# Optimization experiments

Hardware: AMD Instinct MI355X
Metric: run time of the kernel (lower is better)

Reference implementation:

```python
import jax, jax.numpy as jnp
import numpy as np
from jax import lax

SOFTPLUS_THRESHOLD = 20.0

def _softplus_thresh(z):
    # softplus(z, beta=1, threshold=20): linear above threshold
    return jnp.where(z > SOFTPLUS_THRESHOLD, z,
                     jnp.log1p(jnp.exp(jnp.minimum(z, SOFTPLUS_THRESHOLD))))

def setup_inputs() -> dict:
    key = jax.random.key(0)
    ks = jax.random.split(key, 8)
    L, E, R, N = 512, 5120, 160, 16
    scale = 0.02
    x = jax.random.normal(ks[0], (1, 1, L, E), dtype=jnp.float32)
    W_dt_low = jax.random.normal(ks[1], (E, R), dtype=jnp.float32) * scale
    W_dt = jax.random.normal(ks[2], (R, E), dtype=jnp.float32) * scale
    dt_bias = jax.random.normal(ks[3], (E,), dtype=jnp.float32) * scale
    W_B = jax.random.normal(ks[4], (E, N), dtype=jnp.float32) * scale
    W_C = jax.random.normal(ks[5], (E, N), dtype=jnp.float32) * scale
    # A_log ~ log of positive values so A = -exp(A_log) is a stable decay
    A_log = jnp.log(1.0 + jax.random.uniform(ks[6], (E, N), dtype=jnp.float32) * 15.0)
    D = jax.random.normal(ks[7], (E,), dtype=jnp.float32)
    return {"x": x, "W_dt_low": W_dt_low, "W_dt": W_dt, "dt_bias": dt_bias,
            "W_B": W_B, "W_C": W_C, "A_log": A_log, "D": D}

def reference(x, W_dt_low, W_dt, dt_bias, W_B, W_C, A_log, D):
    orig_shape = x.shape              # [1,1,L,E]
    L, E = orig_shape[-2], orig_shape[-1]
    xf = x.reshape(L, E)
    # delta_t: x -> dt_rank -> d_inner, then thresholded softplus
    delta = _softplus_thresh((xf @ W_dt_low) @ W_dt + dt_bias)   # [L,E]
    A = -jnp.exp(A_log)                                          # [E,N]
    # discretization: abar = exp(delta * A), bbar = delta * B * x
    abar = jnp.exp(delta[:, :, None] * A[None])                  # [L,E,N]
    B = xf @ W_B                                                 # [L,N]
    bbar = delta[:, :, None] * B[:, None, :] * xf[:, :, None]    # [L,E,N]
    # linear recurrence h_t = abar_t * h_{t-1} + bbar_t via associative scan
    def combine(c1, c2):
        a1, b1 = c1
        a2, b2 = c2
        return a1 * a2, a2 * b1 + b2
    _, h = lax.associative_scan(combine, (abar, bbar), axis=0)   # [L,E,N]
    C = xf @ W_C                                                 # [L,N]
    y = jnp.einsum('len,ln->le', h, C)                           # hc_sum_reduce
    out = xf * D + y
    return out.reshape(orig_shape)
```

## Files before the change

### kernel.cpp

```cpp
#include <hip/hip_runtime.h>
#include <math.h>

#define LL 512
#define EE 5120
#define RR 160
#define NS 16
#define NTOT 192
#define KS 32
#define KCHUNK 160
#define CH 16
#define NC 32

#define XCONV_BLOCKS 1280
#define WALL_TILES   960
#define WDT_TILES    800

typedef __attribute__((ext_vector_type(8))) short short8;
typedef __attribute__((ext_vector_type(4))) short short4v;
typedef __attribute__((ext_vector_type(4))) float f32x4;

__device__ inline float softplus_t(float z) {
    return z > 20.f ? z : log1pf(__expf(fminf(z, 20.f)));
}

__device__ inline short f2bf(float f) {
    unsigned u = __float_as_uint(f);
    unsigned r = (u + 0x7FFFu + ((u >> 16) & 1u)) >> 16;
    return (short)r;
}

__device__ inline float bf2f(unsigned short u) {
    return __uint_as_float(((unsigned)u) << 16);
}

__global__ __launch_bounds__(256) void prep_kernel(
        const float* __restrict__ x,
        const float* __restrict__ Wlow,
        const float* __restrict__ WB,
        const float* __restrict__ WC,
        const float* __restrict__ Wdt,
        short* __restrict__ xb,
        short* __restrict__ WallT,
        short* __restrict__ WdtT) {
    const int tid = threadIdx.x;
    const int bid = blockIdx.x;
    if (bid < XCONV_BLOCKS) {
        size_t base = (size_t)bid * 2048 + (size_t)tid * 8;
        float4 v0 = *reinterpret_cast<const float4*>(x + base);
        float4 v1 = *reinterpret_cast<const float4*>(x + base + 4);
        short8 o;
        o[0] = f2bf(v0.x); o[1] = f2bf(v0.y); o[2] = f2bf(v0.z); o[3] = f2bf(v0.w);
        o[4] = f2bf(v1.x); o[5] = f2bf(v1.y); o[6] = f2bf(v1.z); o[7] = f2bf(v1.w);
        *reinterpret_cast<short8*>(xb + base) = o;
        return;
    }
    __shared__ float tile[32][33];
    const int row = tid >> 3, col4 = (tid & 7) * 4;
    if (bid < XCONV_BLOCKS + WALL_TILES) {
        const int t = bid - XCONV_BLOCKS;
        const int k0 = (t / 6) * 32, n0 = (t % 6) * 32;
#pragma unroll
        for (int i = 0; i < 4; ++i) {
            int n = n0 + col4 + i, k = k0 + row;
            float v;
            if (n < RR)            v = Wlow[(size_t)k * RR + n];
            else if (n < RR + NS)  v = WB[(size_t)k * NS + (n - RR)];
            else                   v = WC[(size_t)k * NS + (n - RR - NS)];
            tile[row][col4 + i] = v;
        }
        __syncthreads();
        const int nr = tid >> 3, kc = (tid & 7) * 4;
        short4v o;
#pragma unroll
        for (int i = 0; i < 4; ++i) o[i] = f2bf(tile[kc + i][nr]);
        *reinterpret_cast<short4v*>(WallT + (size_t)(n0 + nr) * EE + k0 + kc) = o;
    } else {
        const int t = bid - XCONV_BLOCKS - WALL_TILES;
        const int n0 = (t / 5) * 32, k0 = (t % 5) * 32;
#pragma unroll
        for (int i = 0; i < 4; ++i)
            tile[row][col4 + i] = Wdt[(size_t)(k0 + row) * EE + n0 + col4 + i];
        __syncthreads();
        const int nr = tid >> 3, kc = (tid & 7) * 4;
        short4v o;
#pragma unroll
        for (int i = 0; i < 4; ++i) o[i] = f2bf(tile[kc + i][nr]);
        *reinterpret_cast<short4v*>(WdtT + (size_t)(n0 + nr) * RR + k0 + kc) = o;
    }
}

__global__ __launch_bounds__(256) void g1m_kernel(
        const short* __restrict__ xb,
        const short* __restrict__ WallT,
        short* __restrict__ part) {
    const int tid = threadIdx.x;
    const int w = tid >> 6, l = tid & 63;
    const int wm = w >> 1, wn = w & 1;
    const int m0 = blockIdx.x * 64 + wm * 32;
    const int n0 = blockIdx.y * 64 + wn * 32;
    const int kz = blockIdx.z;
    const int row16 = l & 15, kg = (l >> 4) * 8;
    f32x4 acc[2][2] = {};
    const short* ap0 = xb + (size_t)(m0 + row16) * EE + kz * KCHUNK + kg;
    const short* ap1 = ap0 + (size_t)16 * EE;
    const short* bp0 = WallT + (size_t)(n0 + row16) * EE + kz * KCHUNK + kg;
    const short* bp1 = bp0 + (size_t)16 * EE;
#pragma unroll
    for (int s = 0; s < KCHUNK / 32; ++s) {
        short8 a0 = *reinterpret_cast<const short8*>(ap0 + s * 32);
        short8 a1 = *reinterpret_cast<const short8*>(ap1 + s * 32);
        short8 b0 = *reinterpret_cast<const short8*>(bp0 + s * 32);
        short8 b1 = *reinterpret_cast<const short8*>(bp1 + s * 32);
        acc[0][0] = __builtin_amdgcn_mfma_f32_16x16x32_bf16(a0, b0, acc[0][0], 0, 0, 0);
        acc[0][1] = __builtin_amdgcn_mfma_f32_16x16x32_bf16(a0, b1, acc[0][1], 0, 0, 0);
        acc[1][0] = __builtin_amdgcn_mfma_f32_16x16x32_bf16(a1, b0, acc[1][0], 0, 0, 0);
        acc[1][1] = __builtin_amdgcn_mfma_f32_16x16x32_bf16(a1, b1, acc[1][1], 0, 0, 0);
    }
    const int r0 = (l >> 4) * 4;
    const int c = l & 15;
#pragma unroll
    for (int i = 0; i < 2; ++i)
#pragma unroll
        for (int j = 0; j < 2; ++j) {
            size_t base = ((size_t)kz * LL + (m0 + i * 16 + r0)) * NTOT + (n0 + j * 16 + c);
            part[base]            = f2bf(acc[i][j][0]);
            part[base + NTOT]     = f2bf(acc[i][j][1]);
            part[base + 2 * NTOT] = f2bf(acc[i][j][2]);
            part[base + 3 * NTOT] = f2bf(acc[i][j][3]);
        }
}

__global__ __launch_bounds__(256) void r1_kernel(
        const short* __restrict__ part,
        short* __restrict__ tmpb,
        float* __restrict__ Bb,
        float* __restrict__ Cb) {
    int idx = blockIdx.x * 256 + threadIdx.x;
    int m = idx / NTOT, j = idx % NTOT;
    float s = 0.f;
#pragma unroll
    for (int ks = 0; ks < KS; ++ks)
        s += bf2f((unsigned short)part[(size_t)ks * LL * NTOT + idx]);
    if (j < RR) tmpb[m * RR + j] = f2bf(s);
    else if (j < RR + NS) Bb[m * NS + (j - RR)] = s;
    else Cb[m * NS + (j - RR - NS)] = s;
}

__device__ inline void delta_tile(
        const short* __restrict__ tmpb,
        const short* __restrict__ WdtT,
        const float* __restrict__ bias,
        int t0, int e0, int tid,
        float (*d_lds)[257]) {
    const int w = tid >> 6, l = tid & 63;
    const int row16 = l & 15, koff = (l >> 4) * 8;
    f32x4 acc[4] = {};
    const short* bp = tmpb + (size_t)(t0 + row16) * RR + koff;
    const short* ap = WdtT + (size_t)(e0 + w * 64 + row16) * RR + koff;
#pragma unroll
    for (int s = 0; s < 5; ++s) {
        short8 b0 = *reinterpret_cast<const short8*>(bp + s * 32);
#pragma unroll
        for (int ef = 0; ef < 4; ++ef) {
            short8 a0 = *reinterpret_cast<const short8*>(ap + (size_t)ef * 16 * RR + s * 32);
            acc[ef] = __builtin_amdgcn_mfma_f32_16x16x32_bf16(a0, b0, acc[ef], 0, 0, 0);
        }
    }
    const int r0 = (l >> 4) * 4, tl = l & 15;
#pragma unroll
    for (int ef = 0; ef < 4; ++ef) {
#pragma unroll
        for (int r = 0; r < 4; ++r) {
            int el = w * 64 + ef * 16 + r0 + r;
            float dv = softplus_t(acc[ef][r] + bias[e0 + el]);
            d_lds[tl][el] = bf2f((unsigned short)f2bf(dv));
        }
    }
}

__global__ __launch_bounds__(256) void passAf_kernel(
        const short* __restrict__ tmpb,
        const short* __restrict__ WdtT,
        const float* __restrict__ bias,
        const unsigned short* __restrict__ xb,
        const float* __restrict__ Bb,
        const float* __restrict__ A_log,
        unsigned short* __restrict__ deltab,
        unsigned short* __restrict__ Hloc,
        float* __restrict__ sumd) {
    __shared__ float d_lds[CH][257];
    __shared__ unsigned short x_lds[CH][264];
    __shared__ float b_lds[CH][NS];
    const int c = blockIdx.y;
    const int e0 = blockIdx.x * 256;
    const int tid = threadIdx.x;
    const int t0 = c * CH;

    b_lds[tid >> 4][tid & 15] = Bb[t0 * NS + tid];
#pragma unroll
    for (int v = tid; v < CH * 32; v += 256) {
        int ttv = v >> 5, ee = (v & 31) * 8;
        short8 xv8 = *reinterpret_cast<const short8*>(xb + (size_t)(t0 + ttv) * EE + e0 + ee);
        *reinterpret_cast<short8*>(&x_lds[ttv][ee]) = xv8;
    }
    delta_tile(tmpb, WdtT, bias, t0, e0, tid, d_lds);
    __syncthreads();

    const int e = e0 + tid;
    float Ac[NS];
#pragma unroll
    for (int q = 0; q < 4; ++q) {
        float4 al = *reinterpret_cast<const float4*>(&A_log[(size_t)e * NS + q * 4]);
        Ac[q * 4 + 0] = -__expf(al.x);
        Ac[q * 4 + 1] = -__expf(al.y);
        Ac[q * 4 + 2] = -__expf(al.z);
        Ac[q * 4 + 3] = -__expf(al.w);
    }
    float h[NS];
#pragma unroll
    for (int n = 0; n < NS; ++n) h[n] = 0.f;
    float sd = 0.f;

#pragma unroll
    for (int tt = 0; tt < CH; ++tt) {
        float d = d_lds[tt][tid];
        deltab[(size_t)(t0 + tt) * EE + e] = (unsigned short)f2bf(d);
        float xv = bf2f(x_lds[tt][tid]);
        sd += d;
        float bx = d * xv;
#pragma unroll
        for (int n = 0; n < NS; ++n) {
            float a = __expf(d * Ac[n]);
            h[n] = a * h[n] + bx * b_lds[tt][n];
        }
    }
    size_t base = ((size_t)c * EE + e) * NS;
    short8 p0, p1;
#pragma unroll
    for (int n = 0; n < 8; ++n) { p0[n] = f2bf(h[n]); p1[n] = f2bf(h[n + 8]); }
    *reinterpret_cast<short8*>(Hloc + base)     = p0;
    *reinterpret_cast<short8*>(Hloc + base + 8) = p1;
    sumd[(size_t)c * EE + e] = sd;
}

__global__ __launch_bounds__(256) void passB_kernel(
        const unsigned short* __restrict__ Hloc,
        const float* __restrict__ sumd,
        const float* __restrict__ A_log,
        unsigned short* __restrict__ Hstart) {
    const int wk = blockIdx.x * 256 + threadIdx.x;
    const int eB = wk >> 4;
    const float AcB = -__expf(A_log[wk]);
    float hs = 0.f;
#pragma unroll
    for (int cc = 0; cc < NC; ++cc) {
        size_t off = (size_t)cc * EE * NS + wk;
        Hstart[off] = (unsigned short)f2bf(hs);
        hs = __expf(AcB * sumd[(size_t)cc * EE + eB]) * hs + bf2f(Hloc[off]);
    }
}

__global__ __launch_bounds__(256) void passC_kernel(
        const unsigned short* __restrict__ deltab,
        const unsigned short* __restrict__ xb,
        const float* __restrict__ Bb,
        const float* __restrict__ Cb,
        const float* __restrict__ A_log,
        const float* __restrict__ Dvec,
        const unsigned short* __restrict__ Hstart,
        float* __restrict__ out) {
    __shared__ unsigned short dl_lds[CH][264];
    __shared__ unsigned short x_lds[CH][264];
    __shared__ float b_lds[CH][NS];
    __shared__ float c_lds[CH][NS];
    const int c = blockIdx.y;
    const int e0 = blockIdx.x * 256;
    const int tid = threadIdx.x;
    const int t0 = c * CH;

    b_lds[tid >> 4][tid & 15] = Bb[t0 * NS + tid];
    c_lds[tid >> 4][tid & 15] = Cb[t0 * NS + tid];
#pragma unroll
    for (int v = tid; v < CH * 32; v += 256) {
        int ttv = v >> 5, ee = (v & 31) * 8;
        size_t g = (size_t)(t0 + ttv) * EE + e0 + ee;
        *reinterpret_cast<short8*>(&dl_lds[ttv][ee]) =
            *reinterpret_cast<const short8*>(deltab + g);
        *reinterpret_cast<short8*>(&x_lds[ttv][ee]) =
            *reinterpret_cast<const short8*>(xb + g);
    }
    __syncthreads();

    const int e = e0 + tid;
    float Ac[NS];
#pragma unroll
    for (int q = 0; q < 4; ++q) {
        float4 al = *reinterpret_cast<const float4*>(&A_log[(size_t)e * NS + q * 4]);
        Ac[q * 4 + 0] = -__expf(al.x);
        Ac[q * 4 + 1] = -__expf(al.y);
        Ac[q * 4 + 2] = -__expf(al.z);
        Ac[q * 4 + 3] = -__expf(al.w);
    }
    float h[NS];
    size_t base = ((size_t)c * EE + e) * NS;
    {
        short8 p0 = *reinterpret_cast<const short8*>(Hstart + base);
        short8 p1 = *reinterpret_cast<const short8*>(Hstart + base + 8);
#pragma unroll
        for (int n = 0; n < 8; ++n) {
            h[n]     = bf2f((unsigned short)p0[n]);
            h[n + 8] = bf2f((unsigned short)p1[n]);
        }
    }
    const float Dval = Dvec[e];

#pragma unroll
    for (int tt = 0; tt < CH; ++tt) {
        float d  = bf2f(dl_lds[tt][tid]);
        float xv = bf2f(x_lds[tt][tid]);
        float bx = d * xv;
        float y = 0.f;
#pragma unroll
        for (int n = 0; n < NS; ++n) {
            float a = __expf(d * Ac[n]);
            h[n] = a * h[n] + bx * b_lds[tt][n];
            y += h[n] * c_lds[tt][n];
        }
        out[(size_t)(t0 + tt) * EE + e] = xv * Dval + y;
    }
}

extern "C" void kernel_launch(void* const* d_in, const int* in_sizes, int n_in,
                              void* d_out, int out_size, void* d_ws, size_t ws_size,
                              hipStream_t stream) {
    const float* x     = (const float*)d_in[0];
    const float* Wlow  = (const float*)d_in[1];
    const float* Wdt   = (const float*)d_in[2];
    const float* bias  = (const float*)d_in[3];
    const float* WB    = (const float*)d_in[4];
    const float* WC    = (const float*)d_in[5];
    const float* Alog  = (const float*)d_in[6];
    const float* Dv    = (const float*)d_in[7];
    float* out = (float*)d_out;
    float* wsf = (float*)d_ws;

    float*          Bb     = wsf;
    float*          Cb     = wsf + 8192;
    short*          WallT  = (short*)(wsf + 16384);
    short*          WdtT   = (short*)(wsf + 507904);
    short*          tmpb   = (short*)(wsf + 917504);
    short*          xb     = (short*)(wsf + 958464);
    short*          part   = (short*)(wsf + 2269184);
    unsigned short* deltab = (unsigned short*)(wsf + 3842048);
    unsigned short* Hloc   = (unsigned short*)(wsf + 5152768);
    unsigned short* Hstart = (unsigned short*)(wsf + 6463488);
    float*          sumd   = wsf + 7774208;

    prep_kernel<<<dim3(XCONV_BLOCKS + WALL_TILES + WDT_TILES), 256, 0, stream>>>(
        x, Wlow, WB, WC, Wdt, xb, WallT, WdtT);
    g1m_kernel<<<dim3(8, 3, KS), 256, 0, stream>>>(xb, WallT, part);
    r1_kernel<<<dim3(384), 256, 0, stream>>>(part, tmpb, Bb, Cb);
    passAf_kernel<<<dim3(EE / 256, NC), 256, 0, stream>>>(
        tmpb, WdtT, bias, (const unsigned short*)xb, Bb, Alog, deltab, Hloc, sumd);
    passB_kernel<<<dim3((EE * NS) / 256), 256, 0, stream>>>(Hloc, sumd, Alog, Hstart);
    passC_kernel<<<dim3(EE / 256, NC), 256, 0, stream>>>(
        (const unsigned short*)deltab, (const unsigned short*)xb, Bb, Cb, Alog, Dv,
        Hstart, out);
}
```

Before: 69.34 us.

## Compute local chunk outputs in pass A and correct with carried state in pass C

Pass A now accumulates the chunk-local output y (from a zero initial state) and the running cumulative delta, and stores both as bf16 instead of storing delta. Pass C no longer reruns the recurrence. It adds the contribution of the carried-in state as sum_n C*Hs*exp(cumdelta*A). This removes the B-term FMAs and the serial h dependency from pass C, at the cost of one extra bf16 stream written and read. It also adds bf16 rounding of the cumulative delta inside an exponent, which may cost accuracy.

```diff
diff --git a/kernel.cpp b/kernel.cpp
--- a/kernel.cpp
+++ b/kernel.cpp
@@ -184,19 +184,23 @@
         const float* __restrict__ bias,
         const unsigned short* __restrict__ xb,
         const float* __restrict__ Bb,
+        const float* __restrict__ Cb,
         const float* __restrict__ A_log,
-        unsigned short* __restrict__ deltab,
         unsigned short* __restrict__ Hloc,
-        float* __restrict__ sumd) {
+        float* __restrict__ sumd,
+        unsigned short* __restrict__ ylocb,
+        unsigned short* __restrict__ cumdb) {
     __shared__ float d_lds[CH][257];
     __shared__ unsigned short x_lds[CH][264];
     __shared__ float b_lds[CH][NS];
+    __shared__ float c_lds[CH][NS];
     const int c = blockIdx.y;
     const int e0 = blockIdx.x * 256;
     const int tid = threadIdx.x;
     const int t0 = c * CH;
 
     b_lds[tid >> 4][tid & 15] = Bb[t0 * NS + tid];
+    c_lds[tid >> 4][tid & 15] = Cb[t0 * NS + tid];
 #pragma unroll
     for (int v = tid; v < CH * 32; v += 256) {
         int ttv = v >> 5, ee = (v & 31) * 8;
@@ -224,15 +228,19 @@
 #pragma unroll
     for (int tt = 0; tt < CH; ++tt) {
         float d = d_lds[tt][tid];
-        deltab[(size_t)(t0 + tt) * EE + e] = (unsigned short)f2bf(d);
         float xv = bf2f(x_lds[tt][tid]);
         sd += d;
         float bx = d * xv;
+        float yv = 0.f;
 #pragma unroll
         for (int n = 0; n < NS; ++n) {
             float a = __expf(d * Ac[n]);
             h[n] = a * h[n] + bx * b_lds[tt][n];
-        }
+            yv += h[n] * c_lds[tt][n];
+        }
+        size_t idx = (size_t)(t0 + tt) * EE + e;
+        ylocb[idx] = (unsigned short)f2bf(yv);
+        cumdb[idx] = (unsigned short)f2bf(sd);
     }
     size_t base = ((size_t)c * EE + e) * NS;
     short8 p0, p1;
@@ -261,31 +269,32 @@
 }
 
 __global__ __launch_bounds__(256) void passC_kernel(
-        const unsigned short* __restrict__ deltab,
+        const unsigned short* __restrict__ ylocb,
+        const unsigned short* __restrict__ cumdb,
         const unsigned short* __restrict__ xb,
-        const float* __restrict__ Bb,
         const float* __restrict__ Cb,
         const float* __restrict__ A_log,
         const float* __restrict__ Dvec,
         const unsigned short* __restrict__ Hstart,
         float* __restrict__ out) {
-    __shared__ unsigned short dl_lds[CH][264];
+    __shared__ unsigned short yl_lds[CH][264];
+    __shared__ unsigned short cd_lds[CH][264];
     __shared__ unsigned short x_lds[CH][264];
-    __shared__ float b_lds[CH][NS];
     __shared__ float c_lds[CH][NS];
     const int c = blockIdx.y;
     const int e0 = blockIdx.x * 256;
     const int tid = threadIdx.x;
     const int t0 = c * CH;
 
-    b_lds[tid >> 4][tid & 15] = Bb[t0 * NS + tid];
     c_lds[tid >> 4][tid & 15] = Cb[t0 * NS + tid];
 #pragma unroll
     for (int v = tid; v < CH * 32; v += 256) {
         int ttv = v >> 5, ee = (v & 31) * 8;
         size_t g = (size_t)(t0 + ttv) * EE + e0 + ee;
-        *reinterpret_cast<short8*>(&dl_lds[ttv][ee]) =
-            *reinterpret_cast<const short8*>(deltab + g);
+        *reinterpret_cast<short8*>(&yl_lds[ttv][ee]) =
+            *reinterpret_cast<const short8*>(ylocb + g);
+        *reinterpret_cast<short8*>(&cd_lds[ttv][ee]) =
+            *reinterpret_cast<const short8*>(cumdb + g);
         *reinterpret_cast<short8*>(&x_lds[ttv][ee]) =
             *reinterpret_cast<const short8*>(xb + g);
     }
@@ -301,31 +310,27 @@
         Ac[q * 4 + 2] = -__expf(al.z);
         Ac[q * 4 + 3] = -__expf(al.w);
     }
-    float h[NS];
-    size_t base = ((size_t)c * EE + e) * NS;
+    float Hs[NS];
     {
+        size_t base = ((size_t)c * EE + e) * NS;
         short8 p0 = *reinterpret_cast<const short8*>(Hstart + base);
         short8 p1 = *reinterpret_cast<const short8*>(Hstart + base + 8);
 #pragma unroll
         for (int n = 0; n < 8; ++n) {
-            h[n]     = bf2f((unsigned short)p0[n]);
-            h[n + 8] = bf2f((unsigned short)p1[n]);
+            Hs[n]     = bf2f((unsigned short)p0[n]);
+            Hs[n + 8] = bf2f((unsigned short)p1[n]);
         }
     }
     const float Dval = Dvec[e];
 
 #pragma unroll
     for (int tt = 0; tt < CH; ++tt) {
-        float d  = bf2f(dl_lds[tt][tid]);
+        float y  = bf2f(yl_lds[tt][tid]);
+        float cd = bf2f(cd_lds[tt][tid]);
         float xv = bf2f(x_lds[tt][tid]);
-        float bx = d * xv;
-        float y = 0.f;
-#pragma unroll
-        for (int n = 0; n < NS; ++n) {
-            float a = __expf(d * Ac[n]);
-            h[n] = a * h[n] + bx * b_lds[tt][n];
-            y += h[n] * c_lds[tt][n];
-        }
+#pragma unroll
+        for (int n = 0; n < NS; ++n)
+            y += c_lds[tt][n] * (Hs[n] * __expf(cd * Ac[n]));
         out[(size_t)(t0 + tt) * EE + e] = xv * Dval + y;
     }
 }
@@ -351,19 +356,20 @@
     short*          tmpb   = (short*)(wsf + 917504);
     short*          xb     = (short*)(wsf + 958464);
     short*          part   = (short*)(wsf + 2269184);
-    unsigned short* deltab = (unsigned short*)(wsf + 3842048);
+    unsigned short* ylocb  = (unsigned short*)(wsf + 3842048);
     unsigned short* Hloc   = (unsigned short*)(wsf + 5152768);
     unsigned short* Hstart = (unsigned short*)(wsf + 6463488);
-    float*          sumd   = wsf + 7774208;
+    unsigned short* cumdb  = (unsigned short*)(wsf + 7774208);
+    float*          sumd   = wsf + 9084928;
 
     prep_kernel<<<dim3(XCONV_BLOCKS + WALL_TILES + WDT_TILES), 256, 0, stream>>>(
         x, Wlow, WB, WC, Wdt, xb, WallT, WdtT);
     g1m_kernel<<<dim3(8, 3, KS), 256, 0, stream>>>(xb, WallT, part);
     r1_kernel<<<dim3(384), 256, 0, stream>>>(part, tmpb, Bb, Cb);
     passAf_kernel<<<dim3(EE / 256, NC), 256, 0, stream>>>(
-        tmpb, WdtT, bias, (const unsigned short*)xb, Bb, Alog, deltab, Hloc, sumd);
+        tmpb, WdtT, bias, (const unsigned short*)xb, Bb, Cb, Alog,
+        Hloc, sumd, ylocb, cumdb);
     passB_kernel<<<dim3((EE * NS) / 256), 256, 0, stream>>>(Hloc, sumd, Alog, Hstart);
     passC_kernel<<<dim3(EE / 256, NC), 256, 0, stream>>>(
-        (const unsigned short*)deltab, (const unsigned short*)xb, Bb, Cb, Alog, Dv,
-        Hstart, out);
-}
+        ylocb, cumdb, (const unsigned short*)xb, Cb, Alog, Dv, Hstart, out);
+}
```

Result: no change. 70.12 us (+1.1%).
